# Optimization experiments

Measured on AMD Instinct MI355X. Metric: run time of the kernel, lower is better.

The kernel has to match this reference:

```python
import jax, jax.numpy as jnp
import numpy as np

N, E = 8000, 96000
S, V, G = 128, 64, 64          # scalar channels, l=1 vector channels, gate channels
LAT, OH = 128, 64
D = S + 3 * V                  # 320 feature dim per node/edge
AVG_NEIGH = 12.0
EPS = 1e-8

def _split(x):
    return x[:, :S], x[:, S:].reshape(x.shape[0], V, 3)

def sep_layernorm(x, ws, bs, wv):
    # separable LN: layernorm on l=0 scalars, component RMS norm on l=1 vectors
    s, v = _split(x)
    mu = jnp.mean(s, -1, keepdims=True)
    sc = s - mu
    s = sc * jax.lax.rsqrt(jnp.mean(sc * sc, -1, keepdims=True) + EPS) * ws + bs
    v = v * jax.lax.rsqrt(jnp.mean(v * v, (-2, -1), keepdims=True) + EPS) * wv[:, None]
    return s, v

def edge_frame(ev):
    # orthonormal frame with first axis along the edge (SO2 m=0 axis)
    a = ev * jax.lax.rsqrt(jnp.sum(ev * ev, -1, keepdims=True) + EPS)
    ref = jnp.where(jnp.abs(a[:, :1]) < 0.9,
                    jnp.array([1.0, 0.0, 0.0], ev.dtype),
                    jnp.array([0.0, 1.0, 0.0], ev.dtype))
    b = jnp.cross(a, ref)
    b = b * jax.lax.rsqrt(jnp.sum(b * b, -1, keepdims=True) + EPS)
    c = jnp.cross(a, b)
    return jnp.stack([a, b, c], axis=1)  # [E,3,3], rows are frame axes

def gate_act(s_all, v, n_s, n_g):
    s, g = s_all[:, :n_s], s_all[:, n_s:n_s + n_g]
    return jax.nn.silu(s), jax.nn.sigmoid(g)[:, :, None] * v

def e3_linear(s, v, ws, bs, wv):
    s = s @ ws * (1.0 / np.sqrt(s.shape[-1])) + bs
    v = jnp.einsum('eum,uk->ekm', v, wv) * (1.0 / np.sqrt(v.shape[1]))
    return s, v

def setup_inputs() -> dict:
    key = jax.random.key(0)
    ks = jax.random.split(key, 20)
    f = jnp.float32
    p = lambda k, sh: jax.random.normal(k, sh, f)
    inp = {}
    inp['latents'] = p(ks[0], (E, LAT))
    inp['node_features'] = p(ks[1], (N, D))
    inp['edge_features'] = p(ks[2], (E, D))
    at = jax.random.randint(ks[3], (N,), 0, OH)
    inp['atom_type'] = at
    inp['node_onehot'] = jax.nn.one_hot(at, OH, dtype=f)
    inp['edge_index'] = jax.random.randint(ks[4], (2, E), 0, N)
    inp['edge_vector'] = p(ks[5], (E, 3))
    inp['active_edges'] = jnp.arange(E)
    inp['sln_n_ws'] = jnp.ones((S,), f); inp['sln_n_bs'] = jnp.zeros((S,), f); inp['sln_n_wv'] = jnp.ones((V,), f)
    inp['sln_e_ws'] = jnp.ones((S,), f); inp['sln_e_bs'] = jnp.zeros((S,), f); inp['sln_e_wv'] = jnp.ones((V,), f)
    inp['so2_w0'] = p(ks[6], (3 * S + 3 * V, S + G + V))
    inp['so2_w1r'] = p(ks[7], (3 * V, V))
    inp['so2_w1i'] = p(ks[8], (3 * V, V))
    inp['env_w'] = p(ks[9], (LAT, S + V))
    inp['lp_ws'] = p(ks[10], (S, S)); inp['lp_bs'] = jnp.zeros((S,), f); inp['lp_wv'] = p(ks[11], (V, V))
    inp['oh_w_ss'] = p(ks[12], (S, OH, S))
    inp['oh_w_sg'] = p(ks[13], (S, OH, G))
    inp['oh_w_vv'] = p(ks[14], (V, OH, V))
    inp['ohl_ws'] = p(ks[15], (S, S)); inp['ohl_bs'] = jnp.zeros((S,), f); inp['ohl_wv'] = p(ks[16], (V, V))
    inp['res_param'] = jnp.zeros((1,), f)
    return inp

def reference(latents, node_features, edge_features, atom_type, node_onehot,
              edge_index, edge_vector, active_edges,
              sln_n_ws, sln_n_bs, sln_n_wv, sln_e_ws, sln_e_bs, sln_e_wv,
              so2_w0, so2_w1r, so2_w1i, env_w,
              lp_ws, lp_bs, lp_wv,
              oh_w_ss, oh_w_sg, oh_w_vv, ohl_ws, ohl_bs, ohl_wv, res_param):
    ctr = edge_index[0][active_edges]
    nbr = edge_index[1][active_edges]
    ns, nv = sep_layernorm(node_features, sln_n_ws, sln_n_bs, sln_n_wv)
    es, evf = sep_layernorm(edge_features, sln_e_ws, sln_e_bs, sln_e_wv)
    # concat center | edge | neighbor (scalars and vectors kept separate)
    sc = jnp.concatenate([ns[ctr], es, ns[nbr]], -1)          # [E, 3S]
    vc = jnp.concatenate([nv[ctr], evf, nv[nbr]], 1)          # [E, 3V, 3]
    R = edge_frame(edge_vector[active_edges])
    vf = jnp.einsum('eij,euj->eui', R, vc)                    # rotate into edge frame
    # SO2 linear: m=0 mixes scalars + on-axis components; m=+-1 mix with (re,im) weights
    m0_in = jnp.concatenate([sc, vf[:, :, 0]], -1)            # [E, 3S+3V]
    m0_out = m0_in @ so2_w0 * (1.0 / np.sqrt(m0_in.shape[-1]))  # [E, S+G+V]
    n1 = 1.0 / np.sqrt(vf.shape[1])
    vp = (vf[:, :, 1] @ so2_w1r - vf[:, :, 2] @ so2_w1i) * n1
    vm = (vf[:, :, 1] @ so2_w1i + vf[:, :, 2] @ so2_w1r) * n1
    v_out = jnp.stack([m0_out[:, S + G:], vp, vm], -1)        # [E,V,3] in frame
    v_out = jnp.einsum('eij,eui->euj', R, v_out)              # rotate back
    # gate activation + post linear
    ms, mv = gate_act(m0_out[:, :S + G], v_out, S, G)
    ms, mv = e3_linear(ms, mv, lp_ws, lp_bs, lp_wv)
    # env weighting (E3ElementLinear with weights from latents) + scatter to centers
    w = latents[active_edges] @ env_w * (1.0 / np.sqrt(LAT))  # [E, S+V]
    ms = ms * w[:, :S]
    mv = mv * w[:, S:, None]
    inv = 1.0 / np.sqrt(AVG_NEIGH)
    agg_s = jax.ops.segment_sum(ms, ctr, num_segments=N) * inv
    agg_v = jax.ops.segment_sum(mv, ctr, num_segments=N) * inv
    # one-hot FullyConnectedTensorProduct -> gate -> linear
    n_ss = 1.0 / np.sqrt(S * OH)
    n_vv = 1.0 / np.sqrt(V * OH)
    t_s = jnp.einsum('nu,nv,uvk->nk', agg_s, node_onehot, oh_w_ss) * n_ss
    t_g = jnp.einsum('nu,nv,uvk->nk', agg_s, node_onehot, oh_w_sg) * n_ss
    t_v = jnp.einsum('num,nv,uvk->nkm', agg_v, node_onehot, oh_w_vv) * n_vv
    gs, gv = gate_act(jnp.concatenate([t_s, t_g], -1), t_v, S, G)
    os_, ov = e3_linear(gs, gv, ohl_ws, ohl_bs, ohl_wv)
    new = jnp.concatenate([os_, ov.reshape(-1, 3 * V)], -1)
    # residual mixing (identity residual since node_irreps_in == irreps_out)
    alpha = jax.nn.sigmoid(res_param)[0]
    return alpha * node_features + (1.0 - alpha) * new
```

## Files before the change

### kernel.cpp

```cpp
#include <hip/hip_runtime.h>

#define EPS_LN 1e-8f

typedef __bf16 bf16x8 __attribute__((ext_vector_type(8)));
typedef float  f32x4  __attribute__((ext_vector_type(4)));

__device__ __forceinline__ float sigmoidf_(float x){ return 1.0f/(1.0f+__expf(-x)); }
__device__ __forceinline__ float siluf_(float x){ return x*sigmoidf_(x); }
__device__ __forceinline__ unsigned short f2bf(float x){ union{ __bf16 b; unsigned short u;} c; c.b = (__bf16)x; return c.u; }
__device__ __forceinline__ float bf2f(unsigned short u){ return __uint_as_float(((unsigned)u)<<16); }

union F4 { float4 v; float f[4]; };

__device__ __forceinline__ void st_bf4(char* base, int row, int stride_bytes, int k,
                                       float x0, float x1, float x2, float x3){
    union { __bf16 h[4]; unsigned long long u; } p;
    p.h[0]=(__bf16)x0; p.h[1]=(__bf16)x1; p.h[2]=(__bf16)x2; p.h[3]=(__bf16)x3;
    *(unsigned long long*)(base + row*stride_bytes + ((2*k) ^ ((row&7)<<4))) = p.u;
}
__device__ __forceinline__ bf16x8 ld_frag(const char* base, int row, int stride_bytes, int kbyte){
    return *(const bf16x8*)(base + row*stride_bytes + (kbyte ^ ((row&7)<<4)));
}
__device__ __forceinline__ void st_g4(__bf16* p, float x0, float x1, float x2, float x3){
    union { __bf16 h[4]; unsigned long long u; } pk;
    pk.h[0]=(__bf16)x0; pk.h[1]=(__bf16)x1; pk.h[2]=(__bf16)x2; pk.h[3]=(__bf16)x3;
    *(unsigned long long*)p = pk.u;
}
__device__ __forceinline__ uint4 pack8(float4 a, float4 b){
    union { __bf16 h[8]; uint4 u; } p;
    p.h[0]=(__bf16)a.x; p.h[1]=(__bf16)a.y; p.h[2]=(__bf16)a.z; p.h[3]=(__bf16)a.w;
    p.h[4]=(__bf16)b.x; p.h[5]=(__bf16)b.y; p.h[6]=(__bf16)b.z; p.h[7]=(__bf16)b.w;
    return p.u;
}
__device__ __forceinline__ int fm_idx(int n, int k, int NKT){
    return ((n>>4)*NKT + (k>>5))*512 + ((k>>3)&3)*128 + (n&15)*8 + (k&7);
}

__global__ void prep_all(const float* __restrict__ w0,
                         const float* __restrict__ w1r, const float* __restrict__ w1i,
                         const float* __restrict__ env_w, const float* __restrict__ lp_ws,
                         const float* __restrict__ lp_wv,
                         const float* __restrict__ oh_ss, const float* __restrict__ oh_sg,
                         const float* __restrict__ oh_vv,
                         __bf16* __restrict__ Wt, __bf16* __restrict__ w1rt, __bf16* __restrict__ w1it,
                         __bf16* __restrict__ Wevfm, __bf16* __restrict__ Bnodefm,
                         __bf16* __restrict__ Bvfm,
                         __bf16* __restrict__ envfm, __bf16* __restrict__ lpsfm,
                         __bf16* __restrict__ lpvfm,
                         __bf16* __restrict__ ssT, __bf16* __restrict__ sgT, __bf16* __restrict__ vvT)
{
    int t = blockIdx.x*256 + threadIdx.x;
    if (t < 576*256){
        int n = t/576, k = t%576;
        Wt[t] = (__bf16)w0[(size_t)k*256 + n];
    }
    if (t < 256*320){
        int n = t/320, k = t%320;
        int src = (k<128) ? (128+k) : (384+(k-128));
        Wevfm[fm_idx(n,k,10)] = (__bf16)w0[(size_t)src*256 + n];
    }
    if (t < 512*128){
        int n = t/128, k = t%128;
        float v = (n<256) ? w0[(size_t)k*256 + n] : w0[(size_t)(256+k)*256 + (n-256)];
        Bnodefm[fm_idx(n,k,4)] = (__bf16)v;
    }
    if (t < 64*192){
        int c = t/192, k = t%192;
        w1rt[t] = (__bf16)w1r[(size_t)k*64 + c];
        w1it[t] = (__bf16)w1i[(size_t)k*64 + c];
    }
    if (t < 128*384){
        int n = t/384, k = t%384;
        float v;
        if (n < 64) v = (k<192) ? w1r[(size_t)k*64+n] : -w1i[(size_t)(k-192)*64+n];
        else        v = (k<192) ? w1i[(size_t)k*64+(n-64)] : w1r[(size_t)(k-192)*64+(n-64)];
        Bvfm[fm_idx(n,k,12)] = (__bf16)v;
    }
    if (t < 192*128){ int n=t/128, k=t%128; envfm[fm_idx(n,k,4)] = (__bf16)env_w[(size_t)k*192+n]; }
    if (t < 128*128){ int n=t/128, k=t%128; lpsfm[fm_idx(n,k,4)] = (__bf16)lp_ws[(size_t)k*128+n]; }
    if (t < 64*64)  { int n=t/64,  k=t%64;  lpvfm[fm_idx(n,k,2)] = (__bf16)lp_wv[(size_t)k*64+n]; }
    if (t < 64*128*128){
        int at = t / 16384; int r = t & 16383; int u = r >> 7, k = r & 127;
        ssT[t] = (__bf16)oh_ss[((size_t)u*64 + at)*128 + k];
    }
    if (t < 64*128*64){
        int at = t / 8192; int r = t & 8191; int u = r >> 6, k = r & 63;
        sgT[t] = (__bf16)oh_sg[((size_t)u*64 + at)*64 + k];
    }
    if (t < 64*64*64){
        int at = t / 4096; int r = t & 4095; int u = r >> 6, k = r & 63;
        vvT[t] = (__bf16)oh_vv[((size_t)u*64 + at)*64 + k];
    }
}

__global__ void csr_count(const int* __restrict__ ei, const int* __restrict__ act,
                          int* __restrict__ cnt, int EA)
{
    int e = blockIdx.x*256 + threadIdx.x;
    if (e < EA) atomicAdd(&cnt[ei[act[e]]], 1);
}
__global__ void csr_scan(const int* __restrict__ cnt, int* __restrict__ offs,
                         int* __restrict__ cursor, int N)
{
    __shared__ int part[256];
    int t = threadIdx.x;
    int chunk = (N + 255) / 256;
    int lo = t*chunk, hi = lo+chunk; if (hi > N) hi = N; if (lo > N) lo = N;
    int s = 0;
    for (int i=lo;i<hi;i++) s += cnt[i];
    part[t] = s;
    __syncthreads();
    for (int d=1; d<256; d<<=1){
        int v = (t>=d) ? part[t-d] : 0;
        __syncthreads();
        part[t] += v;
        __syncthreads();
    }
    int run = (t==0) ? 0 : part[t-1];
    for (int i=lo;i<hi;i++){
        offs[i] = run; cursor[i] = run;
        run += cnt[i];
    }
    if (t==255) offs[N] = part[255];
}
__global__ void csr_fill(const int* __restrict__ ei, const int* __restrict__ act,
                         int* __restrict__ cursor, int* __restrict__ elist, int EA)
{
    int e = blockIdx.x*256 + threadIdx.x;
    if (e < EA){
        int n = ei[act[e]];
        int p = atomicAdd(&cursor[n], 1);
        elist[p] = e;
    }
}

__global__ void node_ln_kernel(const float* __restrict__ nf,
                               const float* __restrict__ ws, const float* __restrict__ bs,
                               const float* __restrict__ wv,
                               float* __restrict__ ns, float* __restrict__ nv,
                               __bf16* __restrict__ nsb, int N)
{
    int t = threadIdx.x;
    int lane = t & 63;
    int n = blockIdx.x*4 + (t>>6);
    if (n >= N) return;
    const float* row = nf + (size_t)n*320;
    float s0 = row[lane], s1 = row[64+lane];
    float sum = s0+s1, sq = s0*s0+s1*s1;
    #pragma unroll
    for (int m=1;m<64;m<<=1){ sum += __shfl_xor(sum,m,64); sq += __shfl_xor(sq,m,64); }
    float mu = sum*(1.0f/128.0f);
    float rs = rsqrtf(sq*(1.0f/128.0f) - mu*mu + EPS_LN);
    float o0 = (s0-mu)*rs*ws[lane]    + bs[lane];
    float o1 = (s1-mu)*rs*ws[64+lane] + bs[64+lane];
    ns[(size_t)n*128+lane]    = o0;
    ns[(size_t)n*128+64+lane] = o1;
    nsb[(size_t)n*128+lane]    = (__bf16)o0;
    nsb[(size_t)n*128+64+lane] = (__bf16)o1;
    float v0 = row[128+lane], v1 = row[192+lane], v2 = row[256+lane];
    float vs = v0*v0+v1*v1+v2*v2;
    #pragma unroll
    for (int m=1;m<64;m<<=1) vs += __shfl_xor(vs,m,64);
    float rv = rsqrtf(vs*(1.0f/192.0f) + EPS_LN);
    nv[(size_t)n*192+lane]     = v0*rv*wv[lane/3];
    nv[(size_t)n*192+64+lane]  = v1*rv*wv[(64+lane)/3];
    nv[(size_t)n*192+128+lane] = v2*rv*wv[(128+lane)/3];
}

__global__ void stage_kernel(
    const float* __restrict__ ef_all,
    const int*   __restrict__ edge_index,
    const float* __restrict__ edge_vector,
    const int*   __restrict__ active_edges,
    const float* __restrict__ e_ws, const float* __restrict__ e_bs, const float* __restrict__ e_wv,
    const float* __restrict__ nv,
    __bf16* __restrict__ m0in,
    __bf16* __restrict__ vfg,
    float* __restrict__ Rg, int2* __restrict__ ctnb,
    int EA, int EF)
{
    int tid = blockIdx.x*256 + threadIdx.x;
    int e = tid >> 4, l = tid & 15;
    if (e >= EA) return;
    int ae = active_edges[e];
    int ct = edge_index[ae];
    int nb = edge_index[EF + ae];
    float ex = edge_vector[(size_t)ae*3+0];
    float ey = edge_vector[(size_t)ae*3+1];
    float ez = edge_vector[(size_t)ae*3+2];
    float rn = rsqrtf(ex*ex+ey*ey+ez*ez + EPS_LN);
    float ax = ex*rn, ay = ey*rn, az = ez*rn;
    float rx, ry;
    if (fabsf(ax) < 0.9f) { rx = 1.0f; ry = 0.0f; } else { rx = 0.0f; ry = 1.0f; }
    float bx = -az*ry, by = az*rx, bz = ax*ry - ay*rx;
    float bn = rsqrtf(bx*bx+by*by+bz*bz + EPS_LN);
    bx*=bn; by*=bn; bz*=bn;
    float cx = ay*bz - az*by;
    float cy = az*bx - ax*bz;
    float cz = ax*by - ay*bx;
    if (l == 0){
        float* Rr = Rg + (size_t)e*12;
        *(float4*)(Rr)   = make_float4(ax,ay,az,bx);
        *(float4*)(Rr+4) = make_float4(by,bz,cx,cy);
        *(float4*)(Rr+8) = make_float4(cz,0.f,0.f,0.f);
        ctnb[e] = make_int2(ct, nb);
    }
    __bf16* Arow = m0in + (size_t)e*320;
    __bf16* V1r  = vfg + (size_t)e*384;
    __bf16* V2r  = V1r + 192;
    const float* ef = ef_all + (size_t)e*320;
    {
        F4 sa, sb;
        sa.v = *(const float4*)(ef + l*4);
        sb.v = *(const float4*)(ef + 64 + l*4);
        float sum=0.f, sq=0.f;
        #pragma unroll
        for (int i=0;i<4;i++){ sum += sa.f[i]+sb.f[i]; sq += sa.f[i]*sa.f[i]+sb.f[i]*sb.f[i]; }
        #pragma unroll
        for (int m=1;m<16;m<<=1){ sum += __shfl_xor(sum,m,64); sq += __shfl_xor(sq,m,64); }
        float mu = sum*(1.0f/128.0f);
        float rs = rsqrtf(sq*(1.0f/128.0f)-mu*mu + EPS_LN);
        float o0[4], o1[4];
        #pragma unroll
        for (int i=0;i<4;i++){
            int c0 = l*4+i, c1 = 64+l*4+i;
            o0[i] = (sa.f[i]-mu)*rs*e_ws[c0]+e_bs[c0];
            o1[i] = (sb.f[i]-mu)*rs*e_ws[c1]+e_bs[c1];
        }
        st_g4(Arow + l*4,      o0[0],o0[1],o0[2],o0[3]);
        st_g4(Arow + 64 + l*4, o1[0],o1[1],o1[2],o1[3]);
    }
    {
        F4 va, vb, vc;
        va.v = *(const float4*)(ef + 128 + l*12);
        vb.v = *(const float4*)(ef + 128 + l*12 + 4);
        vc.v = *(const float4*)(ef + 128 + l*12 + 8);
        float vv[12];
        #pragma unroll
        for (int i=0;i<4;i++){ vv[i]=va.f[i]; vv[4+i]=vb.f[i]; vv[8+i]=vc.f[i]; }
        float sq=0.f;
        #pragma unroll
        for (int i=0;i<12;i++) sq += vv[i]*vv[i];
        #pragma unroll
        for (int m=1;m<16;m<<=1) sq += __shfl_xor(sq,m,64);
        float rv = rsqrtf(sq*(1.0f/192.0f) + EPS_LN);
        float f0[4], f1[4], f2[4];
        #pragma unroll
        for (int j=0;j<4;j++){
            int u = 4*l + j;
            float sc = rv * e_wv[u];
            float x = vv[3*j]*sc, y = vv[3*j+1]*sc, z = vv[3*j+2]*sc;
            f0[j] = ax*x+ay*y+az*z;
            f1[j] = bx*x+by*y+bz*z;
            f2[j] = cx*x+cy*y+cz*z;
        }
        st_g4(Arow + 128 + 64 + 4*l, f0[0],f0[1],f0[2],f0[3]);
        st_g4(V1r + 64 + 4*l, f1[0],f1[1],f1[2],f1[3]);
        st_g4(V2r + 64 + 4*l, f2[0],f2[1],f2[2],f2[3]);
    }
    {
        const float* pv = nv + (size_t)ct*192 + l*12;
        F4 va, vb, vc;
        va.v = *(const float4*)(pv);
        vb.v = *(const float4*)(pv+4);
        vc.v = *(const float4*)(pv+8);
        float vv[12];
        #pragma unroll
        for (int i=0;i<4;i++){ vv[i]=va.f[i]; vv[4+i]=vb.f[i]; vv[8+i]=vc.f[i]; }
        float f0[4], f1[4], f2[4];
        #pragma unroll
        for (int j=0;j<4;j++){
            float x = vv[3*j], y = vv[3*j+1], z = vv[3*j+2];
            f0[j] = ax*x+ay*y+az*z;
            f1[j] = bx*x+by*y+bz*z;
            f2[j] = cx*x+cy*y+cz*z;
        }
        st_g4(Arow + 128 + 4*l, f0[0],f0[1],f0[2],f0[3]);
        st_g4(V1r + 4*l, f1[0],f1[1],f1[2],f1[3]);
        st_g4(V2r + 4*l, f2[0],f2[1],f2[2],f2[3]);
    }
    {
        const float* pv = nv + (size_t)nb*192 + l*12;
        F4 va, vb, vc;
        va.v = *(const float4*)(pv);
        vb.v = *(const float4*)(pv+4);
        vc.v = *(const float4*)(pv+8);
        float vv[12];
        #pragma unroll
        for (int i=0;i<4;i++){ vv[i]=va.f[i]; vv[4+i]=vb.f[i]; vv[8+i]=vc.f[i]; }
        float f0[4], f1[4], f2[4];
        #pragma unroll
        for (int j=0;j<4;j++){
            float x = vv[3*j], y = vv[3*j+1], z = vv[3*j+2];
            f0[j] = ax*x+ay*y+az*z;
            f1[j] = bx*x+by*y+bz*z;
            f2[j] = cx*x+cy*y+cz*z;
        }
        st_g4(Arow + 128 + 128 + 4*l, f0[0],f0[1],f0[2],f0[3]);
        st_g4(V1r + 128 + 4*l, f1[0],f1[1],f1[2],f1[3]);
        st_g4(V2r + 128 + 4*l, f2[0],f2[1],f2[2],f2[3]);
    }
}

enum { EPI_PLAIN=0, EPI_LPS=1, EPI_LPV=2 };

template<int N, int K, int RT, int EPI, bool AGATHER>
__global__ __launch_bounds__((N/64)*RT*64)
void gemm_k(const __bf16* __restrict__ Ag, const float* __restrict__ Agf,
            const int* __restrict__ aidx,
            const __bf16* __restrict__ Bfm,
            unsigned short* __restrict__ outp,
            const unsigned short* __restrict__ wenv,
            const float* __restrict__ bias,
            float scale, int M)
{
    constexpr int NT  = N/64;
    constexpr int BM  = RT*64;
    constexpr int T   = NT*RT*64;
    constexpr int NKT = K/32;
    constexpr int NK  = K/64;
    constexpr int NBUF= (NK>1) ? 2 : 1;
    constexpr int CA  = (BM*8 + T - 1)/T;
    __shared__ __align__(16) char lA[NBUF][BM*128];

    const int tid  = threadIdx.x;
    const int brow = blockIdx.x*BM;
    const int mpl  = blockIdx.y;
    const __bf16* A = AGATHER ? nullptr : (Ag + (size_t)mpl*M*K);

    uint4 ra[CA];
    auto loadA = [&](int ks){
        #pragma unroll
        for (int i=0;i<CA;i++){
            int c = tid + i*T;
            if (c < BM*8){
                int r = c>>3;
                int gr = brow + r; if (gr >= M) gr = M-1;
                if constexpr (AGATHER){
                    int ae = aidx[gr];
                    const float* base = Agf + (size_t)ae*K + ks*64 + (c&7)*8;
                    float4 f0 = *(const float4*)(base);
                    float4 f1 = *(const float4*)(base+4);
                    ra[i] = pack8(f0, f1);
                } else {
                    ra[i] = *(const uint4*)((const char*)(A + (size_t)gr*K + ks*64) + (c&7)*16);
                }
            }
        }
    };
    auto storeA = [&](int buf){
        #pragma unroll
        for (int i=0;i<CA;i++){
            int c = tid + i*T;
            if (c < BM*8){
                int r = c>>3, off = (c&7)*16;
                *(uint4*)(&lA[buf][r*128 + (off ^ ((r&7)<<4))]) = ra[i];
            }
        }
    };

    const int wid = tid>>6, ln = tid&63;
    const int cc = ln & 15, gq = ln >> 4;
    const int wn = wid % NT, wm = wid / NT;
    const __bf16* bbase = Bfm + ((size_t)wn*4*NKT)*512 + (size_t)ln*8;

    f32x4 acc[4][4];
    #pragma unroll
    for (int i=0;i<4;i++)
        #pragma unroll
        for (int j=0;j<4;j++) acc[i][j] = (f32x4){0,0,0,0};

    loadA(0); storeA(0);
    int cur = 0;
    for (int ks=0; ks<NK; ks++){
        __syncthreads();
        if (ks+1 < NK) loadA(ks+1);
        #pragma unroll
        for (int kt2=0;kt2<2;kt2++){
            const int kt = ks*2 + kt2;
            const int kb = kt2*64 + 16*gq;
            bf16x8 af[4];
            #pragma unroll
            for (int mf=0;mf<4;mf++){
                int r = wm*64 + mf*16 + cc;
                af[mf] = *(const bf16x8*)(&lA[cur][r*128 + (kb ^ ((r&7)<<4))]);
            }
            #pragma unroll
            for (int nf=0;nf<4;nf++){
                bf16x8 bfr = *(const bf16x8*)(bbase + ((size_t)nf*NKT + kt)*512);
                #pragma unroll
                for (int mf=0;mf<4;mf++)
                    acc[mf][nf] = __builtin_amdgcn_mfma_f32_16x16x32_bf16(af[mf], bfr, acc[mf][nf], 0,0,0);
            }
        }
        if (ks+1 < NK) storeA(cur^1);
        cur ^= (NBUF-1);
    }

    const float inv_avg_ = 0.288675134595f;
    #pragma unroll
    for (int mf=0;mf<4;mf++){
        #pragma unroll
        for (int nf=0;nf<4;nf++){
            #pragma unroll
            for (int j=0;j<4;j++){
                int gr = brow + wm*64 + mf*16 + gq*4 + j;
                if (gr >= M) continue;
                int col = wn*64 + nf*16 + cc;
                float v = acc[mf][nf][j];
                if constexpr (EPI == EPI_PLAIN){
                    outp[(size_t)gr*N + col] = f2bf(v*scale);
                } else if constexpr (EPI == EPI_LPS){
                    float val = (v*scale + bias[col]) * bf2f(wenv[(size_t)gr*192 + col]) * inv_avg_;
                    outp[(size_t)gr*320 + col] = f2bf(val);
                } else {
                    float val = v*0.125f * bf2f(wenv[(size_t)gr*192 + 128 + col]) * inv_avg_;
                    outp[(size_t)gr*320 + 128 + mpl*64 + col] = f2bf(val);
                }
            }
        }
    }
}

__global__ __launch_bounds__(128)
void gemm_lpv(const __bf16* __restrict__ Ag,
              const __bf16* __restrict__ Bfm,
              unsigned short* __restrict__ outp,
              const unsigned short* __restrict__ wenv,
              int M)
{
    constexpr int BM = 128;
    __shared__ __align__(16) char lA[BM*128];

    const int tid  = threadIdx.x;
    const int brow = blockIdx.x*BM;

    uint4 ra[8];
    auto loadA = [&](int pl){
        const __bf16* A = Ag + (size_t)pl*M*64;
        #pragma unroll
        for (int i=0;i<8;i++){
            int c = tid + i*128;
            int r = c>>3;
            int gr = brow + r; if (gr >= M) gr = M-1;
            ra[i] = *(const uint4*)((const char*)(A + (size_t)gr*64) + (c&7)*16);
        }
    };
    auto storeA = [&](){
        #pragma unroll
        for (int i=0;i<8;i++){
            int c = tid + i*128;
            int r = c>>3, off = (c&7)*16;
            *(uint4*)(&lA[r*128 + (off ^ ((r&7)<<4))]) = ra[i];
        }
    };

    const int wid = tid>>6, ln = tid&63;
    const int cc = ln & 15, gq = ln >> 4;
    const int wm = wid;

    bf16x8 bf_[4][2];
    {
        const __bf16* bbase = Bfm + (size_t)ln*8;
        #pragma unroll
        for (int nf=0;nf<4;nf++)
            #pragma unroll
            for (int kt=0;kt<2;kt++)
                bf_[nf][kt] = *(const bf16x8*)(bbase + ((size_t)nf*2 + kt)*512);
    }

    loadA(0); storeA();
    const float inv_avg_ = 0.288675134595f;
    for (int pl=0; pl<3; pl++){
        __syncthreads();
        if (pl < 2) loadA(pl+1);
        f32x4 acc[4][4];
        #pragma unroll
        for (int i=0;i<4;i++)
            #pragma unroll
            for (int j=0;j<4;j++) acc[i][j] = (f32x4){0,0,0,0};
        #pragma unroll
        for (int kt=0;kt<2;kt++){
            const int kb = kt*64 + 16*gq;
            bf16x8 af[4];
            #pragma unroll
            for (int mf=0;mf<4;mf++){
                int r = wm*64 + mf*16 + cc;
                af[mf] = *(const bf16x8*)(&lA[r*128 + (kb ^ ((r&7)<<4))]);
            }
            #pragma unroll
            for (int nf=0;nf<4;nf++)
                #pragma unroll
                for (int mf=0;mf<4;mf++)
                    acc[mf][nf] = __builtin_amdgcn_mfma_f32_16x16x32_bf16(af[mf], bf_[nf][kt], acc[mf][nf], 0,0,0);
        }
        __syncthreads();
        if (pl < 2) storeA();
        #pragma unroll
        for (int mf=0;mf<4;mf++){
            #pragma unroll
            for (int nf=0;nf<4;nf++){
                #pragma unroll
                for (int j=0;j<4;j++){
                    int gr = brow + wm*64 + mf*16 + gq*4 + j;
                    if (gr >= M) continue;
                    int col = nf*16 + cc;
                    float val = acc[mf][nf][j]*0.125f * bf2f(wenv[(size_t)gr*192 + 128 + col]) * inv_avg_;
                    outp[(size_t)gr*320 + 128 + pl*64 + col] = f2bf(val);
                }
            }
        }
    }
}

__global__ void mid_kernel(const unsigned short* __restrict__ m0out,
                           const unsigned short* __restrict__ vpvm,
                           const float* __restrict__ Rg,
                           const int2* __restrict__ ctnb,
                           const __bf16* __restrict__ nodeCN,
                           unsigned short* __restrict__ As,
                           unsigned short* __restrict__ MVp, int EA)
{
    int tid = blockIdx.x*256 + threadIdx.x;
    int e = tid>>6, u = tid&63;
    if (e >= EA) return;
    float rl = (u < 12) ? Rg[(size_t)e*12 + u] : 0.f;
    float R0=__shfl(rl,0,64), R1=__shfl(rl,1,64), R2=__shfl(rl,2,64);
    float R3=__shfl(rl,3,64), R4=__shfl(rl,4,64), R5=__shfl(rl,5,64);
    float R6=__shfl(rl,6,64), R7=__shfl(rl,7,64), R8=__shfl(rl,8,64);
    int2 cn = ctnb[e];
    const __bf16* nct = nodeCN + (size_t)cn.x*512;
    const __bf16* nnb = nodeCN + (size_t)cn.y*512 + 256;
    const float rn0 = 0.0416666666667f;
    float a0 = ((float)nct[u]       + (float)nnb[u])       * rn0;
    float a1 = ((float)nct[64+u]    + (float)nnb[64+u])    * rn0;
    float a2 = ((float)nct[128+u]   + (float)nnb[128+u])   * rn0;
    float a3 = ((float)nct[192+u]   + (float)nnb[192+u])   * rn0;
    const unsigned short* mo = m0out + (size_t)e*256;
    float m0 = bf2f(mo[u])       + a0;
    float m1 = bf2f(mo[64 + u])  + a1;
    float gt = sigmoidf_(bf2f(mo[128 + u]) + a2);
    float s0 = bf2f(mo[192 + u]) + a3;
    float p  = bf2f(vpvm[(size_t)e*128 + u]);
    float q  = bf2f(vpvm[(size_t)e*128 + 64 + u]);
    size_t eu = (size_t)e*64 + u;
    size_t P  = (size_t)EA*64;
    MVp[eu]       = f2bf(gt*(R0*s0 + R3*p + R6*q));
    MVp[P + eu]   = f2bf(gt*(R1*s0 + R4*p + R7*q));
    MVp[2*P + eu] = f2bf(gt*(R2*s0 + R5*p + R8*q));
    As[(size_t)e*128 + u]      = f2bf(siluf_(m0));
    As[(size_t)e*128 + 64 + u] = f2bf(siluf_(m1));
}

__launch_bounds__(256, 3)
__global__ void edge_kernel_fused(
    const float* __restrict__ latents,
    const float* __restrict__ ef_all,
    const int*   __restrict__ edge_index,
    const float* __restrict__ edge_vector,
    const int*   __restrict__ active_edges,
    const float* __restrict__ e_ws, const float* __restrict__ e_bs, const float* __restrict__ e_wv,
    const __bf16* __restrict__ Wt,
    const __bf16* __restrict__ w1rt,
    const __bf16* __restrict__ w1it,
    const float* __restrict__ env_w,
    const float* __restrict__ lp_ws, const float* __restrict__ lp_bs, const float* __restrict__ lp_wv,
    const float* __restrict__ ns, const float* __restrict__ nv,
    unsigned short* __restrict__ eout,
    int EA, int EF)
{
    __shared__ __align__(16) char smem[46592];
    char* sAbC = smem;
    char* sVFC = smem + 18432;
    float* sO  = (float*)smem;
    float* MV  = (float*)(smem + 16640);
    float* WE  = (float*)(smem + 33280);
    float* sR  = (float*)(smem + 45824);

    const int t = threadIdx.x;
    const int g = t >> 4, l = t & 15;
    const int e = blockIdx.x*16 + g;
    const bool act = (e < EA);

    int ct = 0, ae = 0;

    if (act) {
        ae = active_edges[e];
        ct = edge_index[ae];
        int nb = edge_index[EF + ae];
        float ex = edge_vector[(size_t)ae*3+0];
        float ey = edge_vector[(size_t)ae*3+1];
        float ez = edge_vector[(size_t)ae*3+2];
// ... 15 lines not shown
        }
        {
            const float4* pc4 = (const float4*)(ns + (size_t)ct*128);
            const float4* pn4 = (const float4*)(ns + (size_t)nb*128);
            F4 a,b2,c,d;
            a.v = pc4[l]; b2.v = pc4[16+l]; c.v = pn4[l]; d.v = pn4[16+l];
            st_bf4(sAbC, g, 1152, l*4,       a.f[0],a.f[1],a.f[2],a.f[3]);
            st_bf4(sAbC, g, 1152, 64+l*4,    b2.f[0],b2.f[1],b2.f[2],b2.f[3]);
            st_bf4(sAbC, g, 1152, 256+l*4,   c.f[0],c.f[1],c.f[2],c.f[3]);
            st_bf4(sAbC, g, 1152, 320+l*4,   d.f[0],d.f[1],d.f[2],d.f[3]);
        }
        const float* ef = ef_all + (size_t)e*320;
        {
            F4 sa, sb;
            sa.v = *(const float4*)(ef + l*4);
            sb.v = *(const float4*)(ef + 64 + l*4);
            float sum=0.f, sq=0.f;
            #pragma unroll
            for (int i=0;i<4;i++){ sum += sa.f[i]+sb.f[i]; sq += sa.f[i]*sa.f[i]+sb.f[i]*sb.f[i]; }
            #pragma unroll
            for (int m=1;m<16;m<<=1){ sum += __shfl_xor(sum,m,64); sq += __shfl_xor(sq,m,64); }
            float mu = sum*(1.0f/128.0f);
            float rs = rsqrtf(sq*(1.0f/128.0f)-mu*mu + EPS_LN);
            float o0[4], o1[4];
            #pragma unroll
            for (int i=0;i<4;i++){
                int c0 = l*4+i, c1 = 64+l*4+i;
                o0[i] = (sa.f[i]-mu)*rs*e_ws[c0]+e_bs[c0];
                o1[i] = (sb.f[i]-mu)*rs*e_ws[c1]+e_bs[c1];
            }
            st_bf4(sAbC, g, 1152, 128+l*4, o0[0],o0[1],o0[2],o0[3]);
            st_bf4(sAbC, g, 1152, 192+l*4, o1[0],o1[1],o1[2],o1[3]);
        }
        {
            F4 va, vb, vc;
            va.v = *(const float4*)(ef + 128 + l*12);
            vb.v = *(const float4*)(ef + 128 + l*12 + 4);
            vc.v = *(const float4*)(ef + 128 + l*12 + 8);
            float vv[12];
            #pragma unroll
            for (int i=0;i<4;i++){ vv[i]=va.f[i]; vv[4+i]=vb.f[i]; vv[8+i]=vc.f[i]; }
            float sq=0.f;
            #pragma unroll
            for (int i=0;i<12;i++) sq += vv[i]*vv[i];
            #pragma unroll
            for (int m=1;m<16;m<<=1) sq += __shfl_xor(sq,m,64);
            float rv = rsqrtf(sq*(1.0f/192.0f) + EPS_LN);
            float f0[4], f1[4], f2[4];
            #pragma unroll
            for (int j=0;j<4;j++){
                int u = 4*l + j;
                float sc = rv * e_wv[u];
                float x = vv[3*j]*sc, y = vv[3*j+1]*sc, z = vv[3*j+2]*sc;
                f0[j] = ax*x+ay*y+az*z;
                f1[j] = bx*x+by*y+bz*z;
                f2[j] = cx*x+cy*y+cz*z;
            }
            st_bf4(sAbC, g, 1152, 384+64+4*l, f0[0],f0[1],f0[2],f0[3]);
            st_bf4(sVFC, g, 384, 64+4*l, f1[0],f1[1],f1[2],f1[3]);
            st_bf4(sVFC+6144, g, 384, 64+4*l, f2[0],f2[1],f2[2],f2[3]);
        }
        {
            const float* pv = nv + (size_t)ct*192 + l*12;
            F4 va, vb, vc;
            va.v = *(const float4*)(pv);
            vb.v = *(const float4*)(pv+4);
            vc.v = *(const float4*)(pv+8);
            float vv[12];
            #pragma unroll
            for (int i=0;i<4;i++){ vv[i]=va.f[i]; vv[4+i]=vb.f[i]; vv[8+i]=vc.f[i]; }
            float f0[4], f1[4], f2[4];
            #pragma unroll
            for (int j=0;j<4;j++){
                float x = vv[3*j], y = vv[3*j+1], z = vv[3*j+2];
                f0[j] = ax*x+ay*y+az*z;
                f1[j] = bx*x+by*y+bz*z;
                f2[j] = cx*x+cy*y+cz*z;
            }
            st_bf4(sAbC, g, 1152, 384+4*l, f0[0],f0[1],f0[2],f0[3]);
            st_bf4(sVFC, g, 384, 4*l, f1[0],f1[1],f1[2],f1[3]);
            st_bf4(sVFC+6144, g, 384, 4*l, f2[0],f2[1],f2[2],f2[3]);
        }
        {
            const float* pv = nv + (size_t)nb*192 + l*12;
            F4 va, vb, vc;
            va.v = *(const float4*)(pv);
            vb.v = *(const float4*)(pv+4);
            vc.v = *(const float4*)(pv+8);
            float vv[12];
            #pragma unroll
            for (int i=0;i<4;i++){ vv[i]=va.f[i]; vv[4+i]=vb.f[i]; vv[8+i]=vc.f[i]; }
            float f0[4], f1[4], f2[4];
            #pragma unroll
            for (int j=0;j<4;j++){
                float x = vv[3*j], y = vv[3*j+1], z = vv[3*j+2];
                f0[j] = ax*x+ay*y+az*z;
                f1[j] = bx*x+by*y+bz*z;
                f2[j] = cx*x+cy*y+cz*z;
            }
            st_bf4(sAbC, g, 1152, 384+128+4*l, f0[0],f0[1],f0[2],f0[3]);
            st_bf4(sVFC, g, 384, 128+4*l, f1[0],f1[1],f1[2],f1[3]);
            st_bf4(sVFC+6144, g, 384, 128+4*l, f2[0],f2[1],f2[2],f2[3]);
        }
    }
    __syncthreads();

    const int w  = t >> 6;
    const int ln = t & 63;
    const int cc = ln & 15;
    const int gq = ln >> 4;

    f32x4 accM[4] = {{0,0,0,0},{0,0,0,0},{0,0,0,0},{0,0,0,0}};
    {
        const __bf16* wb0 = Wt + (size_t)(64*w + 0  + cc)*576;
        const __bf16* wb1 = Wt + (size_t)(64*w + 16 + cc)*576;
        const __bf16* wb2 = Wt + (size_t)(64*w + 32 + cc)*576;
        const __bf16* wb3 = Wt + (size_t)(64*w + 48 + cc)*576;
        for (int ks=0; ks<18; ks++){
            bf16x8 a = ld_frag(sAbC, cc, 1152, ks*64 + 16*gq);
            int ko = ks*32 + 8*gq;
            bf16x8 b0 = *(const bf16x8*)(wb0 + ko);
            bf16x8 b1 = *(const bf16x8*)(wb1 + ko);
            bf16x8 b2 = *(const bf16x8*)(wb2 + ko);
            bf16x8 b3 = *(const bf16x8*)(wb3 + ko);
            accM[0] = __builtin_amdgcn_mfma_f32_16x16x32_bf16(a, b0, accM[0], 0,0,0);
            accM[1] = __builtin_amdgcn_mfma_f32_16x16x32_bf16(a, b1, accM[1], 0,0,0);
            accM[2] = __builtin_amdgcn_mfma_f32_16x16x32_bf16(a, b2, accM[2], 0,0,0);
            accM[3] = __builtin_amdgcn_mfma_f32_16x16x32_bf16(a, b3, accM[3], 0,0,0);
        }
    }
    f32x4 aP1={0,0,0,0}, aP2={0,0,0,0}, aM1={0,0,0,0}, aM2={0,0,0,0};
    {
        const __bf16* wr = w1rt + (size_t)(16*w + cc)*192;
        const __bf16* wi = w1it + (size_t)(16*w + cc)*192;
        for (int ks=0; ks<6; ks++){
            bf16x8 a1 = ld_frag(sVFC,        cc, 384, ks*64 + 16*gq);
            bf16x8 a2 = ld_frag(sVFC + 6144, cc, 384, ks*64 + 16*gq);
            int ko = ks*32 + 8*gq;
            bf16x8 br = *(const bf16x8*)(wr + ko);
            bf16x8 bi = *(const bf16x8*)(wi + ko);
            aP1 = __builtin_amdgcn_mfma_f32_16x16x32_bf16(a1, br, aP1, 0,0,0);
            aP2 = __builtin_amdgcn_mfma_f32_16x16x32_bf16(a2, bi, aP2, 0,0,0);
            aM1 = __builtin_amdgcn_mfma_f32_16x16x32_bf16(a1, bi, aM1, 0,0,0);
            aM2 = __builtin_amdgcn_mfma_f32_16x16x32_bf16(a2, br, aM2, 0,0,0);
        }
    }
    __syncthreads();

    {
        const float rn0 = 0.0416666666667f;
        #pragma unroll
        for (int jt=0;jt<4;jt++){
            #pragma unroll
            for (int j=0;j<4;j++){
                sO[(gq*4+j)*260 + 64*w + 16*jt + cc] = accM[jt][j]*rn0;
            }
        }
    }
    float vp[4], vm[4];
    {
        const float n1 = 0.0721687836487f;
        #pragma unroll
        for (int j=0;j<4;j++){ vp[j] = (aP1[j]-aP2[j])*n1; vm[j] = (aM1[j]+aM2[j])*n1; }
    }
    __syncthreads();

    {
        int u = w*16 + cc;
        #pragma unroll
        for (int j=0;j<4;j++){
            int er = gq*4 + j;
            if (blockIdx.x*16 + er < EA){
                const float* Rr = &sR[er*12];
                float s0 = sO[er*260 + 192 + u];
                float gt = sigmoidf_(sO[er*260 + 128 + u]);
                float p = vp[j], q = vm[j];
                float4 o;
                o.x = gt*(Rr[0]*s0 + Rr[3]*p + Rr[6]*q);
                o.y = gt*(Rr[1]*s0 + Rr[4]*p + Rr[7]*q);
                o.z = gt*(Rr[2]*s0 + Rr[5]*p + Rr[8]*q);
                o.w = 0.0f;
                *(float4*)&MV[er*260 + u*4] = o;
            }
        }
    }
    if (act) {
        {
            int i0 = l*8;
            F4 oa, ob;
            oa.v = *(const float4*)&sO[g*260 + i0];
            ob.v = *(const float4*)&sO[g*260 + i0 + 4];
            #pragma unroll
            for (int i=0;i<4;i++){ oa.f[i] = siluf_(oa.f[i]); ob.f[i] = siluf_(ob.f[i]); }
            *(float4*)&sO[g*260 + i0]     = oa.v;
            *(float4*)&sO[g*260 + i0 + 4] = ob.v;
        }
        {
            const int cc2 = l*12;
            float wacc[12];
            #pragma unroll
            for (int i=0;i<12;i++) wacc[i]=0.f;
            const float* lat = latents + (size_t)ae*128;
            for (int k=0;k<128;k+=4){
                F4 la;
                la.v = *(const float4*)(lat + k);
                #pragma unroll
                for (int kk=0;kk<4;kk++){
                    const float* er_ = env_w + (size_t)(k+kk)*192 + cc2;
                    F4 e0v,e1v,e2v;
                    e0v.v = *(const float4*)(er_);
                    e1v.v = *(const float4*)(er_+4);
                    e2v.v = *(const float4*)(er_+8);
                    #pragma unroll
                    for (int i=0;i<4;i++){
                        wacc[i]   += la.f[kk]*e0v.f[i];
                        wacc[4+i] += la.f[kk]*e1v.f[i];
                        wacc[8+i] += la.f[kk]*e2v.f[i];
                    }
                }
            }
            const float inv128 = 0.0883883476483f;
            #pragma unroll
            for (int i=0;i<12;i++) WE[g*196 + cc2 + i] = wacc[i]*inv128;
        }
    }
    __syncthreads();

    if (act) {
        const float inv_avg = 0.288675134595f;
        unsigned short* orow = eout + (size_t)e*320;
        {
            int c0 = l*8;
            float a8[8];
            #pragma unroll
            for (int i=0;i<8;i++) a8[i]=0.f;
            for (int k=0;k<128;k+=4){
                F4 av;
                av.v = *(const float4*)&sO[g*260 + k];
                #pragma unroll
                for (int kk=0;kk<4;kk++){
                    const float* wr = lp_ws + (size_t)(k+kk)*128 + c0;
                    F4 w0, w1_;
                    w0.v  = *(const float4*)(wr);
                    w1_.v = *(const float4*)(wr+4);
                    #pragma unroll
                    for (int i=0;i<4;i++){ a8[i] += av.f[kk]*w0.f[i]; a8[4+i] += av.f[kk]*w1_.f[i]; }
                }
            }
            const float s128 = 0.0883883476483f;
            union { unsigned short h[8]; uint4 u; } ps;
            #pragma unroll
            for (int i=0;i<8;i++){
                int c = c0+i;
                ps.h[i] = f2bf((a8[i]*s128 + lp_bs[c]) * WE[g*196 + c] * inv_avg);
            }
            *(uint4*)(orow + c0) = ps.u;
        }
        {
            int k0 = l*4;
            float av[4][3];
            #pragma unroll
            for (int j=0;j<4;j++)
                #pragma unroll
                for (int m2=0;m2<3;m2++) av[j][m2]=0.f;
            for (int u=0;u<64;u++){
                F4 wv4, mv4;
                wv4.v = *(const float4*)(lp_wv + (size_t)u*64 + k0);
                mv4.v = *(const float4*)&MV[g*260 + u*4];
                #pragma unroll
                for (int j=0;j<4;j++){
                    av[j][0] += wv4.f[j]*mv4.f[0];
                    av[j][1] += wv4.f[j]*mv4.f[1];
                    av[j][2] += wv4.f[j]*mv4.f[2];
                }
            }
            #pragma unroll
            for (int j=0;j<4;j++){
                int k = k0+j;
                float wk = WE[g*196 + 128 + k] * 0.125f * inv_avg;
                orow[128 +       k] = f2bf(av[j][0]*wk);
                orow[128 + 64  + k] = f2bf(av[j][1]*wk);
                orow[128 + 128 + k] = f2bf(av[j][2]*wk);
            }
        }
    }
}

__global__ void node_out_kernel(
    const float* __restrict__ nf,
    const int* __restrict__ atom_type,
    const int* __restrict__ offs, const int* __restrict__ elist,
    const unsigned short* __restrict__ eout,
    const __bf16* __restrict__ ssT, const __bf16* __restrict__ sgT, const __bf16* __restrict__ vvT,
    const float* __restrict__ ohl_ws, const float* __restrict__ ohl_bs, const float* __restrict__ ohl_wv,
    const float* __restrict__ res_param,
    float* __restrict__ out, int N)
{
    __shared__ int   sE[64];
    __shared__ float AGS[128];
    __shared__ float AGV[192];
    __shared__ float TSs[128];
    __shared__ float SG[64];
    __shared__ float TV[192];
    const int n = blockIdx.x;
    const int t = threadIdx.x;
    const int at = atom_type[n];
    const int lo = offs[n], hi = offs[n+1];

    float aLo = 0.f, aHi = 0.f;
    for (int base = lo; base < hi; base += 64){
        int cnt = hi - base; if (cnt > 64) cnt = 64;
        __syncthreads();
        if (t < cnt) sE[t] = elist[base + t];
        __syncthreads();
        if (t < 160){
            int i = 0;
            for (; i+4 <= cnt; i += 4){
                unsigned x0 = *(const unsigned*)(eout + (size_t)sE[i  ]*320 + 2*t);
                unsigned x1 = *(const unsigned*)(eout + (size_t)sE[i+1]*320 + 2*t);
                unsigned x2 = *(const unsigned*)(eout + (size_t)sE[i+2]*320 + 2*t);
                unsigned x3 = *(const unsigned*)(eout + (size_t)sE[i+3]*320 + 2*t);
                aLo += bf2f((unsigned short)x0) + bf2f((unsigned short)x1)
                     + bf2f((unsigned short)x2) + bf2f((unsigned short)x3);
                aHi += bf2f((unsigned short)(x0>>16)) + bf2f((unsigned short)(x1>>16))
                     + bf2f((unsigned short)(x2>>16)) + bf2f((unsigned short)(x3>>16));
            }
            for (; i < cnt; i++){
                unsigned x = *(const unsigned*)(eout + (size_t)sE[i]*320 + 2*t);
                aLo += bf2f((unsigned short)x);
                aHi += bf2f((unsigned short)(x>>16));
            }
        }
    }
    if (t < 160){
        int c0 = 2*t, c1 = 2*t+1;
        if (c0 < 128) AGS[c0] = aLo; else { int d=c0-128; AGV[(d&63)*3 + (d>>6)] = aLo; }
        if (c1 < 128) AGS[c1] = aHi; else { int d=c1-128; AGV[(d&63)*3 + (d>>6)] = aHi; }
    }
    __syncthreads();
    const float n_ss = 0.0110485434560f;
    const float n_vv = 0.015625f;
    if (t < 128) {
        const __bf16* w = ssT + (size_t)at*16384 + t;
        float acc = 0.0f;
        #pragma unroll 8
        for (int u=0;u<128;u++) acc += AGS[u]*(float)w[(size_t)u*128];
        TSs[t] = siluf_(acc*n_ss);
    } else if (t < 192) {
        int k = t-128;
        const __bf16* w = sgT + (size_t)at*8192 + k;
        float acc = 0.0f;
        #pragma unroll 8
        for (int u=0;u<128;u++) acc += AGS[u]*(float)w[(size_t)u*64];
        SG[k] = sigmoidf_(acc*n_ss);
    } else {
        int k = t-192;
        const __bf16* w = vvT + (size_t)at*4096 + k;
        float a0=0,a1=0,a2=0;
        #pragma unroll 8
        for (int u=0;u<64;u++){
            float wv = (float)w[(size_t)u*64];
            a0 += AGV[u*3+0]*wv;
            a1 += AGV[u*3+1]*wv;
            a2 += AGV[u*3+2]*wv;
        }
        TV[k*3+0]=a0*n_vv; TV[k*3+1]=a1*n_vv; TV[k*3+2]=a2*n_vv;
    }
    __syncthreads();
    const float alpha = sigmoidf_(res_param[0]);
    const float beta  = 1.0f - alpha;
    if (t < 128) {
        float acc = 0.0f;
        #pragma unroll 8
        for (int k=0;k<128;k++) acc += TSs[k]*ohl_ws[(size_t)k*128 + t];
        float val = acc*0.0883883476483f + ohl_bs[t];
        out[(size_t)n*320 + t] = alpha*nf[(size_t)n*320 + t] + beta*val;
    } else if (t >= 192) {
        int k = t-192;
        float a0=0,a1=0,a2=0;
        #pragma unroll 8
        for (int u=0;u<64;u++){
            float w = ohl_wv[(size_t)u*64 + k]*SG[u];
            a0 += TV[u*3+0]*w; a1 += TV[u*3+1]*w; a2 += TV[u*3+2]*w;
        }
        size_t base = (size_t)n*320 + 128 + (size_t)k*3;
        out[base+0] = alpha*nf[base+0] + beta*(a0*0.125f);
        out[base+1] = alpha*nf[base+1] + beta*(a1*0.125f);
        out[base+2] = alpha*nf[base+2] + beta*(a2*0.125f);
    }
}

extern "C" void kernel_launch(void* const* d_in, const int* in_sizes, int n_in,
                              void* d_out, int out_size, void* d_ws, size_t ws_size,
                              hipStream_t stream)
{
    const float* latents       = (const float*)d_in[0];
    const float* node_features = (const float*)d_in[1];
    const float* edge_features = (const float*)d_in[2];
    const int*   atom_type     = (const int*)d_in[3];
    const int*   edge_index    = (const int*)d_in[5];
    const float* edge_vector   = (const float*)d_in[6];
    const int*   active_edges  = (const int*)d_in[7];
    const float* sln_n_ws = (const float*)d_in[8];
    const float* sln_n_bs = (const float*)d_in[9];
    const float* sln_n_wv = (const float*)d_in[10];
    const float* sln_e_ws = (const float*)d_in[11];
    const float* sln_e_bs = (const float*)d_in[12];
    const float* sln_e_wv = (const float*)d_in[13];
    const float* so2_w0   = (const float*)d_in[14];
    const float* so2_w1r  = (const float*)d_in[15];
    const float* so2_w1i  = (const float*)d_in[16];
    const float* env_w    = (const float*)d_in[17];
    const float* lp_ws    = (const float*)d_in[18];
    const float* lp_bs    = (const float*)d_in[19];
    const float* lp_wv    = (const float*)d_in[20];
    const float* oh_w_ss  = (const float*)d_in[21];
    const float* oh_w_sg  = (const float*)d_in[22];
    const float* oh_w_vv  = (const float*)d_in[23];
    const float* ohl_ws   = (const float*)d_in[24];
    const float* ohl_bs   = (const float*)d_in[25];
    const float* ohl_wv   = (const float*)d_in[26];
    const float* res_param= (const float*)d_in[27];
    float* out = (float*)d_out;

    const int N  = in_sizes[1] / 320;
    const int EF = in_sizes[5] / 2;
    const int EA = in_sizes[7];

    char* p = (char*)d_ws;
    auto alloc = [&](size_t bytes) -> char* {
        char* r = p; p += (bytes + 255) & ~(size_t)255; return r;
    };
    float* ns      = (float*)alloc((size_t)N*128*4);
    float* nv      = (float*)alloc((size_t)N*192*4);
    __bf16* nsb    = (__bf16*)alloc((size_t)N*128*2);
    int*   cnt     = (int*)  alloc((size_t)N*4);
    int*   offs    = (int*)  alloc(((size_t)N+1)*4);
    int*   cursor  = (int*)  alloc((size_t)N*4);
    int*   elist   = (int*)  alloc((size_t)EA*4);
    __bf16* Wt     = (__bf16*)alloc((size_t)576*256*2);
    __bf16* w1rt   = (__bf16*)alloc((size_t)64*192*2);
    __bf16* w1it   = (__bf16*)alloc((size_t)64*192*2);
    __bf16* Wevfm  = (__bf16*)alloc((size_t)256*320*2);
    __bf16* Bnodefm= (__bf16*)alloc((size_t)512*128*2);
    __bf16* Bvfm   = (__bf16*)alloc((size_t)128*384*2);
    __bf16* envfm  = (__bf16*)alloc((size_t)192*128*2);
    __bf16* lpsfm  = (__bf16*)alloc((size_t)128*128*2);
    __bf16* lpvfm  = (__bf16*)alloc((size_t)64*64*2);
    __bf16* ssT    = (__bf16*)alloc((size_t)64*128*128*2);
    __bf16* sgT    = (__bf16*)alloc((size_t)64*128*64*2);
    __bf16* vvT    = (__bf16*)alloc((size_t)64*64*64*2);
    __bf16* nodeCN = (__bf16*)alloc((size_t)N*512*2);
    int2*  ctnb    = (int2*) alloc((size_t)EA*8);
    unsigned short* eout = (unsigned short*)alloc((size_t)EA*320*2);
    unsigned short* w_env= (unsigned short*)alloc((size_t)EA*192*2);
    float*  Rg    = (float*) alloc((size_t)EA*12*4);
    __bf16* m0in  = (__bf16*)alloc((size_t)EA*320*2);
    __bf16* vfg   = (__bf16*)alloc((size_t)EA*384*2);
    size_t split_need = (size_t)(p - (char*)d_ws);
    const bool use_split = (split_need <= ws_size);

    unsigned short* vpvm  = eout;
    unsigned short* m0out = (unsigned short*)vfg;
    unsigned short* As    = (unsigned short*)m0in;
    unsigned short* MVp   = As + (size_t)EA*128;

    hipMemsetAsync(cnt, 0, (size_t)N*sizeof(int), stream);
    prep_all<<<4096, 256, 0, stream>>>(so2_w0, so2_w1r, so2_w1i, env_w, lp_ws, lp_wv,
                                       oh_w_ss, oh_w_sg, oh_w_vv,
                                       Wt, w1rt, w1it, Wevfm, Bnodefm, Bvfm,
                                       envfm, lpsfm, lpvfm, ssT, sgT, vvT);
    node_ln_kernel<<<(N+3)/4, 256, 0, stream>>>(node_features, sln_n_ws, sln_n_bs, sln_n_wv, ns, nv, nsb, N);
    csr_count<<<(EA+255)/256, 256, 0, stream>>>(edge_index, active_edges, cnt, EA);
    csr_scan<<<1, 256, 0, stream>>>(cnt, offs, cursor, N);
    csr_fill<<<(EA+255)/256, 256, 0, stream>>>(edge_index, active_edges, cursor, elist, EA);

    const float rn0    = 0.0416666666667f;
    const float n1     = 0.0721687836487f;
    const float inv128 = 0.0883883476483f;

    if (use_split){
        const int NB64  = (EA + 63) / 64;
        const int NB128 = (EA + 127) / 128;
        const int NBn   = (N + 63) / 64;
        gemm_k<512,128,1,EPI_PLAIN,false><<<dim3(NBn,1), 512, 0, stream>>>(
            nsb, nullptr, nullptr, Bnodefm, (unsigned short*)nodeCN, nullptr, nullptr, 1.0f, N);
        stage_kernel<<<(EA+15)/16, 256, 0, stream>>>(edge_features, edge_index, edge_vector, active_edges,
            sln_e_ws, sln_e_bs, sln_e_wv, nv, m0in, vfg, Rg, ctnb, EA, EF);
        gemm_k<128,384,2,EPI_PLAIN,false><<<dim3(NB128,1), 256, 0, stream>>>(
            vfg, nullptr, nullptr, Bvfm, vpvm, nullptr, nullptr, n1, EA);
        gemm_k<256,320,1,EPI_PLAIN,false><<<dim3(NB64,1), 256, 0, stream>>>(
            m0in, nullptr, nullptr, Wevfm, m0out, nullptr, nullptr, rn0, EA);
        mid_kernel<<<(EA*64+255)/256, 256, 0, stream>>>(m0out, vpvm, Rg, ctnb, nodeCN, As, MVp, EA);
        gemm_k<192,128,1,EPI_PLAIN,true><<<dim3(NB64,1), 192, 0, stream>>>(
            nullptr, latents, active_edges, envfm, w_env, nullptr, nullptr, inv128, EA);
        gemm_k<128,128,2,EPI_LPS,false><<<dim3(NB128,1), 256, 0, stream>>>(
            (const __bf16*)As, nullptr, nullptr, lpsfm, eout, w_env, lp_bs, inv128, EA);
        gemm_lpv<<<NB128, 128, 0, stream>>>(
            (const __bf16*)MVp, lpvfm, eout, w_env, EA);
    } else {
        edge_kernel_fused<<<(EA+15)/16, 256, 0, stream>>>(latents, edge_features, edge_index, edge_vector, active_edges,
            sln_e_ws, sln_e_bs, sln_e_wv, Wt, w1rt, w1it, env_w, lp_ws, lp_bs, lp_wv,
            ns, nv, eout, EA, EF);
    }
    node_out_kernel<<<N, 256, 0, stream>>>(node_features, atom_type, offs, elist, eout,
        ssT, sgT, vvT, ohl_ws, ohl_bs, ohl_wv, res_param, out, N);
}
```

Baseline: 447.7 us.

## Gather bf16 node vectors in stage kernel and split-K node_out one-hot contractions

The node LN kernel now also writes a bf16 copy of the normalized vectors, and the edge staging kernel gathers center and neighbor vectors from that copy, halving gather bytes per edge. Separately, the node_out one-hot tensor-product contraction is restructured so all 256 threads each take a slice of the input channels with paired bf16 weight loads, write partial sums to shared memory, and reduce after a barrier. Previously only one thread per output ran the full serial dot product. This adds a small bf16 write, a shared buffer and an extra sync, plus some precision loss on the gathered vectors.

```diff
diff --git a/kernel.cpp b/kernel.cpp
--- a/kernel.cpp
+++ b/kernel.cpp
@@ -25,6 +25,14 @@
     union { __bf16 h[4]; unsigned long long u; } pk;
     pk.h[0]=(__bf16)x0; pk.h[1]=(__bf16)x1; pk.h[2]=(__bf16)x2; pk.h[3]=(__bf16)x3;
     *(unsigned long long*)p = pk.u;
+}
+__device__ __forceinline__ void ld_bf12(const __bf16* p, float* vv){
+    union { __bf16 h[4]; uint2 u; } a,b,c;
+    a.u = *(const uint2*)(p);
+    b.u = *(const uint2*)(p+4);
+    c.u = *(const uint2*)(p+8);
+    #pragma unroll
+    for (int i=0;i<4;i++){ vv[i]=(float)a.h[i]; vv[4+i]=(float)b.h[i]; vv[8+i]=(float)c.h[i]; }
 }
 __device__ __forceinline__ uint4 pack8(float4 a, float4 b){
     union { __bf16 h[8]; uint4 u; } p;
@@ -138,7 +146,7 @@
                                const float* __restrict__ ws, const float* __restrict__ bs,
                                const float* __restrict__ wv,
                                float* __restrict__ ns, float* __restrict__ nv,
-                               __bf16* __restrict__ nsb, int N)
+                               __bf16* __restrict__ nsb, __bf16* __restrict__ nvb, int N)
 {
     int t = threadIdx.x;
     int lane = t & 63;
@@ -162,9 +170,15 @@
     #pragma unroll
     for (int m=1;m<64;m<<=1) vs += __shfl_xor(vs,m,64);
     float rv = rsqrtf(vs*(1.0f/192.0f) + EPS_LN);
-    nv[(size_t)n*192+lane]     = v0*rv*wv[lane/3];
-    nv[(size_t)n*192+64+lane]  = v1*rv*wv[(64+lane)/3];
-    nv[(size_t)n*192+128+lane] = v2*rv*wv[(128+lane)/3];
+    float nv0 = v0*rv*wv[lane/3];
+    float nv1 = v1*rv*wv[(64+lane)/3];
+    float nv2 = v2*rv*wv[(128+lane)/3];
+    nv[(size_t)n*192+lane]     = nv0;
+    nv[(size_t)n*192+64+lane]  = nv1;
+    nv[(size_t)n*192+128+lane] = nv2;
+    nvb[(size_t)n*192+lane]     = (__bf16)nv0;
+    nvb[(size_t)n*192+64+lane]  = (__bf16)nv1;
+    nvb[(size_t)n*192+128+lane] = (__bf16)nv2;
 }
 
 __global__ void stage_kernel(
@@ -173,7 +187,7 @@
     const float* __restrict__ edge_vector,
     const int*   __restrict__ active_edges,
     const float* __restrict__ e_ws, const float* __restrict__ e_bs, const float* __restrict__ e_wv,
-    const float* __restrict__ nv,
+    const __bf16* __restrict__ nvb,
     __bf16* __restrict__ m0in,
     __bf16* __restrict__ vfg,
     float* __restrict__ Rg, int2* __restrict__ ctnb,
@@ -259,14 +273,8 @@
         st_g4(V2r + 64 + 4*l, f2[0],f2[1],f2[2],f2[3]);
     }
     {
-        const float* pv = nv + (size_t)ct*192 + l*12;
-        F4 va, vb, vc;
-        va.v = *(const float4*)(pv);
-        vb.v = *(const float4*)(pv+4);
-        vc.v = *(const float4*)(pv+8);
         float vv[12];
-        #pragma unroll
-        for (int i=0;i<4;i++){ vv[i]=va.f[i]; vv[4+i]=vb.f[i]; vv[8+i]=vc.f[i]; }
+        ld_bf12(nvb + (size_t)ct*192 + l*12, vv);
         float f0[4], f1[4], f2[4];
         #pragma unroll
         for (int j=0;j<4;j++){
@@ -280,14 +288,8 @@
         st_g4(V2r + 4*l, f2[0],f2[1],f2[2],f2[3]);
     }
     {
-        const float* pv = nv + (size_t)nb*192 + l*12;
-        F4 va, vb, vc;
-        va.v = *(const float4*)(pv);
-        vb.v = *(const float4*)(pv+4);
-        vc.v = *(const float4*)(pv+8);
         float vv[12];
-        #pragma unroll
-        for (int i=0;i<4;i++){ vv[i]=va.f[i]; vv[4+i]=vb.f[i]; vv[8+i]=vc.f[i]; }
+        ld_bf12(nvb + (size_t)nb*192 + l*12, vv);
         float f0[4], f1[4], f2[4];
         #pragma unroll
         for (int j=0;j<4;j++){
@@ -909,6 +911,7 @@
     __shared__ float TSs[128];
     __shared__ float SG[64];
     __shared__ float TV[192];
+    __shared__ float PS[2560];
     const int n = blockIdx.x;
     const int t = threadIdx.x;
     const int at = atom_type[n];
@@ -947,31 +950,70 @@
     __syncthreads();
     const float n_ss = 0.0110485434560f;
     const float n_vv = 0.015625f;
-    if (t < 128) {
-        const __bf16* w = ssT + (size_t)at*16384 + t;
-        float acc = 0.0f;
-        #pragma unroll 8
-        for (int u=0;u<128;u++) acc += AGS[u]*(float)w[(size_t)u*128];
-        TSs[t] = siluf_(acc*n_ss);
-    } else if (t < 192) {
+
+    {
+        int us = t >> 6, kp = t & 63;
+        float aclo = 0.f, achi = 0.f;
+        const __bf16* w = ssT + (size_t)at*16384 + 2*kp;
+        #pragma unroll 4
+        for (int u = us; u < 128; u += 4){
+            unsigned w2 = *(const unsigned*)(w + (size_t)u*128);
+            float a = AGS[u];
+            aclo += a * bf2f((unsigned short)w2);
+            achi += a * bf2f((unsigned short)(w2>>16));
+        }
+        PS[us*128 + 2*kp]   = aclo;
+        PS[us*128 + 2*kp+1] = achi;
+    }
+    {
+        int us = t >> 5, kp = t & 31;
+        float aclo = 0.f, achi = 0.f;
+        const __bf16* w = sgT + (size_t)at*8192 + 2*kp;
+        #pragma unroll 4
+        for (int u = us; u < 128; u += 8){
+            unsigned w2 = *(const unsigned*)(w + (size_t)u*64);
+            float a = AGS[u];
+            aclo += a * bf2f((unsigned short)w2);
+            achi += a * bf2f((unsigned short)(w2>>16));
+        }
+        PS[512 + us*64 + 2*kp]   = aclo;
+        PS[512 + us*64 + 2*kp+1] = achi;
+    }
+    {
+        int us = t >> 5, kp = t & 31;
+        float ac00=0,ac01=0,ac02=0, ac10=0,ac11=0,ac12=0;
+        const __bf16* w = vvT + (size_t)at*4096 + 2*kp;
+        #pragma unroll 2
+        for (int u = us; u < 64; u += 8){
+            unsigned w2 = *(const unsigned*)(w + (size_t)u*64);
+            float w0 = bf2f((unsigned short)w2), w1 = bf2f((unsigned short)(w2>>16));
+            float a0 = AGV[u*3+0], a1 = AGV[u*3+1], a2 = AGV[u*3+2];
+            ac00 += a0*w0; ac01 += a1*w0; ac02 += a2*w0;
+            ac10 += a0*w1; ac11 += a1*w1; ac12 += a2*w1;
+        }
+        float* pv = &PS[1024 + us*192];
+        pv[(2*kp)*3+0]=ac00; pv[(2*kp)*3+1]=ac01; pv[(2*kp)*3+2]=ac02;
+        pv[(2*kp+1)*3+0]=ac10; pv[(2*kp+1)*3+1]=ac11; pv[(2*kp+1)*3+2]=ac12;
+    }
+    __syncthreads();
+    if (t < 128){
+        float s = PS[t] + PS[128+t] + PS[256+t] + PS[384+t];
+        TSs[t] = siluf_(s*n_ss);
+    } else if (t < 192){
         int k = t-128;
-        const __bf16* w = sgT + (size_t)at*8192 + k;
-        float acc = 0.0f;
-        #pragma unroll 8
-        for (int u=0;u<128;u++) acc += AGS[u]*(float)w[(size_t)u*64];
-        SG[k] = sigmoidf_(acc*n_ss);
+        float s = 0.f;
+        #pragma unroll
+        for (int us=0; us<8; us++) s += PS[512 + us*64 + k];
+        SG[k] = sigmoidf_(s*n_ss);
     } else {
         int k = t-192;
-        const __bf16* w = vvT + (size_t)at*4096 + k;
-        float a0=0,a1=0,a2=0;
-        #pragma unroll 8
-        for (int u=0;u<64;u++){
-            float wv = (float)w[(size_t)u*64];
-            a0 += AGV[u*3+0]*wv;
-            a1 += AGV[u*3+1]*wv;
-            a2 += AGV[u*3+2]*wv;
-        }
-        TV[k*3+0]=a0*n_vv; TV[k*3+1]=a1*n_vv; TV[k*3+2]=a2*n_vv;
+        float s0=0,s1=0,s2=0;
+        #pragma unroll
+        for (int us=0; us<8; us++){
+            const float* pv = &PS[1024 + us*192 + k*3];
+            s0 += pv[0]; s1 += pv[1]; s2 += pv[2];
+        }
+        TV[k*3+0]=s0*n_vv; TV[k*3+1]=s1*n_vv; TV[k*3+2]=s2*n_vv;
     }
     __syncthreads();
     const float alpha = sigmoidf_(res_param[0]);
@@ -1041,6 +1083,7 @@
     float* ns      = (float*)alloc((size_t)N*128*4);
     float* nv      = (float*)alloc((size_t)N*192*4);
     __bf16* nsb    = (__bf16*)alloc((size_t)N*128*2);
+    __bf16* nvb    = (__bf16*)alloc((size_t)N*192*2);
     int*   cnt     = (int*)  alloc((size_t)N*4);
     int*   offs    = (int*)  alloc(((size_t)N+1)*4);
     int*   cursor  = (int*)  alloc((size_t)N*4);
@@ -1077,7 +1120,7 @@
                                        oh_w_ss, oh_w_sg, oh_w_vv,
                                        Wt, w1rt, w1it, Wevfm, Bnodefm, Bvfm,
                                        envfm, lpsfm, lpvfm, ssT, sgT, vvT);
-    node_ln_kernel<<<(N+3)/4, 256, 0, stream>>>(node_features, sln_n_ws, sln_n_bs, sln_n_wv, ns, nv, nsb, N);
+    node_ln_kernel<<<(N+3)/4, 256, 0, stream>>>(node_features, sln_n_ws, sln_n_bs, sln_n_wv, ns, nv, nsb, nvb, N);
     csr_count<<<(EA+255)/256, 256, 0, stream>>>(edge_index, active_edges, cnt, EA);
     csr_scan<<<1, 256, 0, stream>>>(cnt, offs, cursor, N);
     csr_fill<<<(EA+255)/256, 256, 0, stream>>>(edge_index, active_edges, cursor, elist, EA);
@@ -1093,7 +1136,7 @@
         gemm_k<512,128,1,EPI_PLAIN,false><<<dim3(NBn,1), 512, 0, stream>>>(
             nsb, nullptr, nullptr, Bnodefm, (unsigned short*)nodeCN, nullptr, nullptr, 1.0f, N);
         stage_kernel<<<(EA+15)/16, 256, 0, stream>>>(edge_features, edge_index, edge_vector, active_edges,
-            sln_e_ws, sln_e_bs, sln_e_wv, nv, m0in, vfg, Rg, ctnb, EA, EF);
+            sln_e_ws, sln_e_bs, sln_e_wv, nvb, m0in, vfg, Rg, ctnb, EA, EF);
         gemm_k<128,384,2,EPI_PLAIN,false><<<dim3(NB128,1), 256, 0, stream>>>(
             vfg, nullptr, nullptr, Bvfm, vpvm, nullptr, nullptr, n1, EA);
         gemm_k<256,320,1,EPI_PLAIN,false><<<dim3(NB64,1), 256, 0, stream>>>(
```

Measured after the change: 443.7 us. Within noise of the previous version (-0.9%).
